# Performance work log

Measured on AMD Instinct MI355X. Metric: run time of the kernel, lower is better.

## Reference

```python
import jax, jax.numpy as jnp
import numpy as np

DMAX = 32
TEMPERATURE = 1.0

B, C, H, T, F = 2, 64, 64, 512, 64


def _windows(x, dmax):
    """x: (..., T, F) -> (..., T, dmax, F); w[..., t, d, :] = x_padded[..., t + d, :],
    where x is zero-padded with dmax-1 frames at the front of T (causal window
    covering frames t-dmax+1 .. t, matching torch ZeroPad2d+Unfold)."""
    Tn = x.shape[-2]
    pad = [(0, 0)] * (x.ndim - 2) + [(dmax - 1, 0), (0, 0)]
    xp = jnp.pad(x, pad)
    idx = jnp.arange(Tn)[:, None] + jnp.arange(dmax)[None, :]  # (T, dmax)
    return xp[..., idx, :]


def setup_inputs() -> dict:
    key = jax.random.key(0)
    ks = jax.random.split(key, 8)
    return {
        "x_mic": jax.random.normal(ks[0], (B, C, T, F), dtype=jnp.float32),
        "x_ref": jax.random.normal(ks[1], (B, C, T, F), dtype=jnp.float32),
        "w_mic": jax.random.normal(ks[2], (H, C), dtype=jnp.float32) * (1.0 / np.sqrt(C)),
        "b_mic": jax.random.normal(ks[3], (H,), dtype=jnp.float32) * 0.01,
        "w_ref": jax.random.normal(ks[4], (H, C), dtype=jnp.float32) * (1.0 / np.sqrt(C)),
        "b_ref": jax.random.normal(ks[5], (H,), dtype=jnp.float32) * 0.01,
        "w_conv": jax.random.normal(ks[6], (1, H, 5, 3), dtype=jnp.float32) * (1.0 / np.sqrt(H * 15)),
        "b_conv": jax.random.normal(ks[7], (1,), dtype=jnp.float32) * 0.01,
    }


def reference(x_mic, x_ref, w_mic, b_mic, w_ref, b_ref, w_conv, b_conv):
    Bn, Cn, Tn, Fn = x_ref.shape
    # 1x1 convs == channel-mixing matmuls
    Q = jnp.einsum('bctf,hc->bhtf', x_mic, w_mic) + b_mic[None, :, None, None]
    K = jnp.einsum('bctf,hc->bhtf', x_ref, w_ref) + b_ref[None, :, None, None]
    # causal sliding windows over T: (B,H,T,dmax,F)
    Kw = _windows(K, DMAX)
    # cross-correlation scores over F: (B,H,T,dmax)
    V = jnp.einsum('bhtf,bhtdf->bhtd', Q, Kw) / jnp.sqrt(jnp.asarray(Fn, jnp.float32))
    # conv over (T, dmax): pad T top by 4 (causal), dmax both sides by 1; kernel (5,3), H->1
    Vp = jnp.pad(V, ((0, 0), (0, 0), (4, 0), (1, 1)))
    Vc = jax.lax.conv_general_dilated(
        Vp, w_conv, window_strides=(1, 1), padding='VALID',
        dimension_numbers=('NCHW', 'OIHW', 'NCHW')) + b_conv[None, :, None, None]
    # delay distribution over dmax
    A = jax.nn.softmax(Vc / TEMPERATURE, axis=-1)  # (B,1,T,dmax)
    # align reference: weighted sum over the causal window
    refw = _windows(x_ref, DMAX)  # (B,C,T,dmax,F)
    aligned = jnp.einsum('btd,bctdf->bctf', A[:, 0], refw)
    return aligned
```

## Files before the change

### kernel.cpp

```cpp
#include <hip/hip_runtime.h>
#include <hip/hip_bf16.h>

#define BB 2
#define CC 64
#define HH 64
#define TT 512
#define FF 64
#define DD 32

typedef short short8 __attribute__((ext_vector_type(8)));
typedef float f32x4  __attribute__((ext_vector_type(4)));

__device__ __forceinline__ unsigned short f2bf(float x) {
    union { float f; unsigned u; } v; v.f = x;
    unsigned r = v.u + 0x7FFFu + ((v.u >> 16) & 1u);
    return (unsigned short)(r >> 16);
}

__global__ __launch_bounds__(256) void k_qk(
    const float* __restrict__ x_mic, const float* __restrict__ x_ref,
    const float* __restrict__ w_mic, const float* __restrict__ b_mic,
    const float* __restrict__ w_ref, const float* __restrict__ b_ref,
    unsigned short* __restrict__ Qb, unsigned short* __restrict__ Kb)
{
    __shared__ unsigned short Wl[64 * 72];
    __shared__ unsigned short Xt[2][64 * 72];
    __shared__ float Bs[64];

    const int tid = threadIdx.x;
    const int b   = blockIdx.x >> 8;
    const int t0  = (blockIdx.x & 255) * 2;
    const int which = blockIdx.y;

    const float* xsrc = which ? x_ref : x_mic;
    const float* wsrc = which ? w_ref : w_mic;
    const float* bsrc = which ? b_ref : b_mic;
    unsigned short* outb = which ? Kb : Qb;

    const int l  = tid & 63;
    const int w  = tid >> 6;
    const int q  = l >> 4;
    const int f4i = l & 15;

    {
        const float4* wg = reinterpret_cast<const float4*>(wsrc);
        const int h  = tid >> 2;
        #pragma unroll
        for (int p = 0; p < 4; ++p) {
            const int c0 = (tid & 3) * 4 + p * 16;
            float4 wv = wg[h * 16 + (c0 >> 2)];
            unsigned w0 = (unsigned)f2bf(wv.x) | ((unsigned)f2bf(wv.y) << 16);
            unsigned w1 = (unsigned)f2bf(wv.z) | ((unsigned)f2bf(wv.w) << 16);
            uint2* dst = reinterpret_cast<uint2*>(&Wl[h * 72 + c0]);
            *dst = make_uint2(w0, w1);
        }
    }
    if (tid < 64) Bs[tid] = bsrc[tid];

    {
        const float4* xg = reinterpret_cast<const float4*>(
            xsrc + (size_t)b * CC * TT * FF);
        #pragma unroll
        for (int t = 0; t < 2; ++t) {
            #pragma unroll
            for (int p = 0; p < 4; ++p) {
                const int cbase = p * 16 + 4 * w;
                const int c     = cbase + q;
                float4 xv = xg[((size_t)c * TT + (t0 + t)) * 16 + f4i];
                float v0 = xv.x, v1 = xv.y, v2 = xv.z, v3 = xv.w;
                float s01 = __shfl_xor((q & 1) ? v0 : v1, 16);
                float s23 = __shfl_xor((q & 1) ? v2 : v3, 16);
                float w0 = (q & 1) ? s01 : v0;
                float w1 = (q & 1) ? v1  : s01;
                float w2 = (q & 1) ? s23 : v2;
                float w3 = (q & 1) ? v3  : s23;
                float r02 = __shfl_xor((q & 2) ? w0 : w2, 32);
                float r13 = __shfl_xor((q & 2) ? w1 : w3, 32);
                float u0 = (q & 2) ? r02 : w0;
                float u1 = (q & 2) ? r13 : w1;
                float u2 = (q & 2) ? w2  : r02;
                float u3 = (q & 2) ? w3  : r13;
                unsigned a0 = (unsigned)f2bf(u0) | ((unsigned)f2bf(u1) << 16);
                unsigned a1 = (unsigned)f2bf(u2) | ((unsigned)f2bf(u3) << 16);
                uint2* dst = reinterpret_cast<uint2*>(
                    &Xt[t][(4 * f4i + q) * 72 + cbase]);
                *dst = make_uint2(a0, a1);
            }
        }
    }
    __syncthreads();

    short8 a0 = *reinterpret_cast<const short8*>(&Wl[(16 * w + f4i) * 72 + q * 8]);
    short8 a1 = *reinterpret_cast<const short8*>(&Wl[(16 * w + f4i) * 72 + (4 + q) * 8]);

    #pragma unroll
    for (int t = 0; t < 2; ++t) {
        f32x4 acc[4];
        #pragma unroll
        for (int n = 0; n < 4; ++n) acc[n] = (f32x4){0.f, 0.f, 0.f, 0.f};

        #pragma unroll
        for (int n = 0; n < 4; ++n) {
            short8 b0 = *reinterpret_cast<const short8*>(
                &Xt[t][(16 * n + f4i) * 72 + q * 8]);
            short8 b1 = *reinterpret_cast<const short8*>(
                &Xt[t][(16 * n + f4i) * 72 + (4 + q) * 8]);
            acc[n] = __builtin_amdgcn_mfma_f32_16x16x32_bf16(a0, b0, acc[n], 0, 0, 0);
            acc[n] = __builtin_amdgcn_mfma_f32_16x16x32_bf16(a1, b1, acc[n], 0, 0, 0);
        }
        #pragma unroll
        for (int n = 0; n < 4; ++n) {
            #pragma unroll
            for (int r = 0; r < 4; ++r) {
                const int h = 16 * w + 4 * q + r;
                const int f = 16 * n + f4i;
                float val = acc[n][r] + Bs[h];
                outb[((size_t)(b * HH + h) * TT + (t0 + t)) * FF + f] = f2bf(val);
            }
        }
    }
}

__global__ __launch_bounds__(256) void k_scores(
    const unsigned short* __restrict__ Qb, const unsigned short* __restrict__ Kb,
    float* __restrict__ V)
{
    __shared__ unsigned short Ql[64 * 72];
    __shared__ unsigned short Kl[96 * 72];

    const int tid = threadIdx.x;
    const int t0  = blockIdx.x * 64;
    const int h   = blockIdx.y, b = blockIdx.z;

    const size_t base = ((size_t)(b * HH + h) * TT) * FF;

    #pragma unroll
    for (int it = 0; it < 5; ++it) {
        int idx = it * 256 + tid;
        if (idx < 512) {
            int r = idx >> 3, g = idx & 7;
            uint4 v = *reinterpret_cast<const uint4*>(Qb + base + (size_t)(t0 + r) * FF + g * 8);
            *reinterpret_cast<uint4*>(&Ql[r * 72 + g * 8]) = v;
        } else {
            int idx2 = idx - 512;
            int r = idx2 >> 3, g = idx2 & 7;
            int j = t0 - 31 + r;
            uint4 v = make_uint4(0u, 0u, 0u, 0u);
            if (j >= 0 && j < TT)
                v = *reinterpret_cast<const uint4*>(Kb + base + (size_t)j * FF + g * 8);
            *reinterpret_cast<uint4*>(&Kl[r * 72 + g * 8]) = v;
        }
    }
    __syncthreads();

    const int l = tid & 63;
    const int w = tid >> 6;
    const int q = l >> 4;
    const int nl = l & 15;

    short8 a0 = *reinterpret_cast<const short8*>(&Ql[(16 * w + nl) * 72 + q * 8]);
    short8 a1 = *reinterpret_cast<const short8*>(&Ql[(16 * w + nl) * 72 + (4 + q) * 8]);

    f32x4 acc[3];
    #pragma unroll
    for (int n = 0; n < 3; ++n) acc[n] = (f32x4){0.f, 0.f, 0.f, 0.f};

    #pragma unroll
    for (int n = 0; n < 3; ++n) {
        short8 b0 = *reinterpret_cast<const short8*>(
            &Kl[(16 * w + 16 * n + nl) * 72 + q * 8]);
        short8 b1 = *reinterpret_cast<const short8*>(
            &Kl[(16 * w + 16 * n + nl) * 72 + (4 + q) * 8]);
        acc[n] = __builtin_amdgcn_mfma_f32_16x16x32_bf16(a0, b0, acc[n], 0, 0, 0);
        acc[n] = __builtin_amdgcn_mfma_f32_16x16x32_bf16(a1, b1, acc[n], 0, 0, 0);
    }

    #pragma unroll
    for (int n = 0; n < 3; ++n) {
        #pragma unroll
        for (int r = 0; r < 4; ++r) {
            const int tloc = 16 * w + 4 * q + r;
            const int d = 16 * n + nl - 4 * q - r;
            if (d >= 0 && d < DD) {
                const int t = t0 + tloc;
                V[((size_t)(b * TT + t) * HH + h) * DD + d] = acc[n][r] * 0.125f;
            }
        }
    }
}

__global__ __launch_bounds__(256) void k_conv_softmax(
    const float* __restrict__ V, const float* __restrict__ wconv,
    const float* __restrict__ bconv, float* __restrict__ A)
{
    __shared__ float Vs[4 + 5 * 2048 + 4];
    __shared__ float wcs[960];
    __shared__ float parts[8 * 32];

    const int tid = threadIdx.x;
    const int t = blockIdx.x, b = blockIdx.y;

    #pragma unroll
    for (int idx = tid; idx < 960; idx += 256) wcs[idx] = wconv[idx];

    const float4* vg = reinterpret_cast<const float4*>(V);
    float4* vs4 = reinterpret_cast<float4*>(Vs);
    #pragma unroll
    for (int idx = tid; idx < 5 * 512; idx += 256) {
        int i = idx >> 9, f4i = idx & 511;
        int tt = t - 4 + i;
        float4 v = make_float4(0.f, 0.f, 0.f, 0.f);
        if (tt >= 0) v = vg[((size_t)(b * TT) + tt) * 512 + f4i];
        vs4[1 + idx] = v;
    }
    __syncthreads();

    const int d  = tid & 31;
    const int hg = tid >> 5;
    float s = 0.f;
    #pragma unroll
    for (int i = 0; i < 5; ++i) {
        #pragma unroll
        for (int hh = 0; hh < 8; ++hh) {
            int h = hg * 8 + hh;
            int base = 4 + i * 2048 + h * 32 + d;
            float vm = Vs[base - 1];  vm = (d > 0)  ? vm : 0.f;
            float v0 = Vs[base];
            float vp = Vs[base + 1];  vp = (d < 31) ? vp : 0.f;
            const float* wr = &wcs[h * 15 + i * 3];
            s += vm * wr[0] + v0 * wr[1] + vp * wr[2];
        }
    }
    parts[hg * 32 + d] = s;
    __syncthreads();

    if (tid < 32) {
        float vc = bconv[0];
        #pragma unroll
        for (int g = 0; g < 8; ++g) vc += parts[g * 32 + tid];
        float m = vc;
        #pragma unroll
        for (int off = 16; off >= 1; off >>= 1) m = fmaxf(m, __shfl_xor(m, off));
        float e = __expf(vc - m);
        float ssum = e;
        #pragma unroll
        for (int off = 16; off >= 1; off >>= 1) ssum += __shfl_xor(ssum, off);
        A[((size_t)(b * TT) + t) * DD + tid] = e / ssum;
    }
}

__global__ __launch_bounds__(256) void k_align(
    const float* __restrict__ x_ref, const float* __restrict__ A, float* __restrict__ out)
{
    __shared__ float Xs[63 * 68];
    __shared__ float As[32 * 33];

    const int tid = threadIdx.x;
    const int t0  = blockIdx.x * 32;
    const int c   = blockIdx.y, b = blockIdx.z;

    const float4* xg = reinterpret_cast<const float4*>(
        x_ref + ((size_t)(b * CC + c) * TT) * FF);
    float4* xs4 = reinterpret_cast<float4*>(Xs);
    #pragma unroll
    for (int idx = tid; idx < 63 * 16; idx += 256) {
        int r = idx >> 4, f4 = idx & 15;
        int tt = t0 - 31 + r;
        float4 v = make_float4(0.f, 0.f, 0.f, 0.f);
        if (tt >= 0) v = xg[tt * 16 + f4];
        xs4[r * 17 + f4] = v;
    }
    #pragma unroll
    for (int idx = tid; idx < 32 * 32; idx += 256) {
        int i = idx >> 5, d = idx & 31;
        As[i * 33 + d] = A[((size_t)(b * TT) + t0 + i) * DD + d];
    }
    __syncthreads();

    const int f4 = tid & 15;
    const int i0 = tid >> 4;
    float4* out4 = reinterpret_cast<float4*>(out);

    #pragma unroll
    for (int pass = 0; pass < 2; ++pass) {
        const int i = i0 + pass * 16;
        float ax = 0.f, ay = 0.f, az = 0.f, aw = 0.f;
        #pragma unroll 8
        for (int d = 0; d < 32; ++d) {
            float a = As[i * 33 + d];
            float4 x = xs4[(i + d) * 17 + f4];
            ax += a * x.x; ay += a * x.y; az += a * x.z; aw += a * x.w;
        }
        out4[((size_t)(b * CC + c) * TT + t0 + i) * 16 + f4] =
            make_float4(ax, ay, az, aw);
    }
}

extern "C" void kernel_launch(void* const* d_in, const int* in_sizes, int n_in,
                              void* d_out, int out_size, void* d_ws, size_t ws_size,
                              hipStream_t stream)
{
    const float* x_mic  = (const float*)d_in[0];
    const float* x_ref  = (const float*)d_in[1];
    const float* w_mic  = (const float*)d_in[2];
    const float* b_mic  = (const float*)d_in[3];
    const float* w_ref  = (const float*)d_in[4];
    const float* b_ref  = (const float*)d_in[5];
    const float* w_conv = (const float*)d_in[6];
    const float* b_conv = (const float*)d_in[7];
    float* out = (float*)d_out;

    unsigned short* Qb = (unsigned short*)d_ws;
    unsigned short* Kb = Qb + 4194304;
    float* V = (float*)(Kb + 4194304);
    float* A = V + 2097152;

    k_qk<<<dim3(BB * (TT / 2), 2), 256, 0, stream>>>(
        x_mic, x_ref, w_mic, b_mic, w_ref, b_ref, Qb, Kb);
    k_scores<<<dim3(TT / 64, HH, BB), 256, 0, stream>>>(Qb, Kb, V);
    k_conv_softmax<<<dim3(TT, BB), 256, 0, stream>>>(V, w_conv, b_conv, A);
    k_align<<<dim3(TT / 32, CC, BB), 256, 0, stream>>>(x_ref, A, out);
}
```

Baseline: 131.8 us.

## Rework QK store layout, batch conv-softmax over timesteps, register-block align kernel

The QK projection now swaps the MFMA operands so each lane holds four consecutive features of one head, which allows packed 8-byte bf16 stores in place of scattered 2-byte stores. Conv+softmax processes four timesteps per block with a padded shared layout, float4 reads, shuffle-based neighbour access and a wave-level reduction, so each block reuses the 8 loaded V rows and drops the second barrier. The align kernel moves to 64-timestep tiles and builds a banded weight matrix in shared memory, so each thread computes a 4x4 register block and the x_ref window reads are amortised. These changes add shared memory use and extra setup for the banded weights, which may lower occupancy.

```diff
diff --git a/kernel.cpp b/kernel.cpp
--- a/kernel.cpp
+++ b/kernel.cpp
@@ -40,7 +40,7 @@
     const int l  = tid & 63;
     const int w  = tid >> 6;
     const int q  = l >> 4;
-    const int f4i = l & 15;
+    const int nl = l & 15;
 
     {
         const float4* wg = reinterpret_cast<const float4*>(wsrc);
@@ -66,7 +66,7 @@
             for (int p = 0; p < 4; ++p) {
                 const int cbase = p * 16 + 4 * w;
                 const int c     = cbase + q;
-                float4 xv = xg[((size_t)c * TT + (t0 + t)) * 16 + f4i];
+                float4 xv = xg[((size_t)c * TT + (t0 + t)) * 16 + nl];
                 float v0 = xv.x, v1 = xv.y, v2 = xv.z, v3 = xv.w;
                 float s01 = __shfl_xor((q & 1) ? v0 : v1, 16);
                 float s23 = __shfl_xor((q & 1) ? v2 : v3, 16);
@@ -83,40 +83,34 @@
                 unsigned a0 = (unsigned)f2bf(u0) | ((unsigned)f2bf(u1) << 16);
                 unsigned a1 = (unsigned)f2bf(u2) | ((unsigned)f2bf(u3) << 16);
                 uint2* dst = reinterpret_cast<uint2*>(
-                    &Xt[t][(4 * f4i + q) * 72 + cbase]);
+                    &Xt[t][(4 * nl + q) * 72 + cbase]);
                 *dst = make_uint2(a0, a1);
             }
         }
     }
     __syncthreads();
 
-    short8 a0 = *reinterpret_cast<const short8*>(&Wl[(16 * w + f4i) * 72 + q * 8]);
-    short8 a1 = *reinterpret_cast<const short8*>(&Wl[(16 * w + f4i) * 72 + (4 + q) * 8]);
+    short8 b0 = *reinterpret_cast<const short8*>(&Wl[(16 * w + nl) * 72 + q * 8]);
+    short8 b1 = *reinterpret_cast<const short8*>(&Wl[(16 * w + nl) * 72 + (4 + q) * 8]);
+    const int h = 16 * w + nl;
+    const float bv = Bs[h];
 
     #pragma unroll
     for (int t = 0; t < 2; ++t) {
-        f32x4 acc[4];
-        #pragma unroll
-        for (int n = 0; n < 4; ++n) acc[n] = (f32x4){0.f, 0.f, 0.f, 0.f};
-
-        #pragma unroll
-        for (int n = 0; n < 4; ++n) {
-            short8 b0 = *reinterpret_cast<const short8*>(
-                &Xt[t][(16 * n + f4i) * 72 + q * 8]);
-            short8 b1 = *reinterpret_cast<const short8*>(
-                &Xt[t][(16 * n + f4i) * 72 + (4 + q) * 8]);
-            acc[n] = __builtin_amdgcn_mfma_f32_16x16x32_bf16(a0, b0, acc[n], 0, 0, 0);
-            acc[n] = __builtin_amdgcn_mfma_f32_16x16x32_bf16(a1, b1, acc[n], 0, 0, 0);
-        }
-        #pragma unroll
-        for (int n = 0; n < 4; ++n) {
-            #pragma unroll
-            for (int r = 0; r < 4; ++r) {
-                const int h = 16 * w + 4 * q + r;
-                const int f = 16 * n + f4i;
-                float val = acc[n][r] + Bs[h];
-                outb[((size_t)(b * HH + h) * TT + (t0 + t)) * FF + f] = f2bf(val);
-            }
+        #pragma unroll
+        for (int mt = 0; mt < 4; ++mt) {
+            f32x4 acc = (f32x4){0.f, 0.f, 0.f, 0.f};
+            short8 a0 = *reinterpret_cast<const short8*>(
+                &Xt[t][(16 * mt + nl) * 72 + q * 8]);
+            short8 a1 = *reinterpret_cast<const short8*>(
+                &Xt[t][(16 * mt + nl) * 72 + (4 + q) * 8]);
+            acc = __builtin_amdgcn_mfma_f32_16x16x32_bf16(a0, b0, acc, 0, 0, 0);
+            acc = __builtin_amdgcn_mfma_f32_16x16x32_bf16(a1, b1, acc, 0, 0, 0);
+            unsigned lo = (unsigned)f2bf(acc[0] + bv) | ((unsigned)f2bf(acc[1] + bv) << 16);
+            unsigned hi = (unsigned)f2bf(acc[2] + bv) | ((unsigned)f2bf(acc[3] + bv) << 16);
+            uint2* dst = reinterpret_cast<uint2*>(
+                &outb[((size_t)(b * HH + h) * TT + (t0 + t)) * FF + 16 * mt + 4 * q]);
+            *dst = make_uint2(lo, hi);
         }
     }
 }
@@ -193,107 +187,153 @@
     const float* __restrict__ V, const float* __restrict__ wconv,
     const float* __restrict__ bconv, float* __restrict__ A)
 {
-    __shared__ float Vs[4 + 5 * 2048 + 4];
+    __shared__ float Vs[8 * 2304];
     __shared__ float wcs[960];
-    __shared__ float parts[8 * 32];
 
     const int tid = threadIdx.x;
-    const int t = blockIdx.x, b = blockIdx.y;
+    const int t0 = blockIdx.x * 4, b = blockIdx.y;
 
     #pragma unroll
     for (int idx = tid; idx < 960; idx += 256) wcs[idx] = wconv[idx];
 
     const float4* vg = reinterpret_cast<const float4*>(V);
-    float4* vs4 = reinterpret_cast<float4*>(Vs);
-    #pragma unroll
-    for (int idx = tid; idx < 5 * 512; idx += 256) {
-        int i = idx >> 9, f4i = idx & 511;
-        int tt = t - 4 + i;
+    #pragma unroll
+    for (int it = 0; it < 16; ++it) {
+        int idx = it * 256 + tid;
+        int r = idx >> 9, g = idx & 511;
+        int h = g >> 3, d4 = g & 7;
+        int tt = t0 - 4 + r;
         float4 v = make_float4(0.f, 0.f, 0.f, 0.f);
-        if (tt >= 0) v = vg[((size_t)(b * TT) + tt) * 512 + f4i];
-        vs4[1 + idx] = v;
-    }
-    __syncthreads();
-
-    const int d  = tid & 31;
-    const int hg = tid >> 5;
-    float s = 0.f;
+        if (tt >= 0) v = vg[((size_t)(b * TT) + tt) * 512 + g];
+        *reinterpret_cast<float4*>(&Vs[r * 2304 + h * 36 + d4 * 4]) = v;
+    }
+    __syncthreads();
+
+    const int dq = tid & 7;
+    const int hg = (tid >> 3) & 7;
+    const int tt = tid >> 6;
+
+    float px = 0.f, py = 0.f, pz = 0.f, pw = 0.f;
     #pragma unroll
     for (int i = 0; i < 5; ++i) {
+        const int r = tt + i;
         #pragma unroll
         for (int hh = 0; hh < 8; ++hh) {
-            int h = hg * 8 + hh;
-            int base = 4 + i * 2048 + h * 32 + d;
-            float vm = Vs[base - 1];  vm = (d > 0)  ? vm : 0.f;
-            float v0 = Vs[base];
-            float vp = Vs[base + 1];  vp = (d < 31) ? vp : 0.f;
-            const float* wr = &wcs[h * 15 + i * 3];
-            s += vm * wr[0] + v0 * wr[1] + vp * wr[2];
-        }
-    }
-    parts[hg * 32 + d] = s;
-    __syncthreads();
-
-    if (tid < 32) {
-        float vc = bconv[0];
-        #pragma unroll
-        for (int g = 0; g < 8; ++g) vc += parts[g * 32 + tid];
-        float m = vc;
-        #pragma unroll
-        for (int off = 16; off >= 1; off >>= 1) m = fmaxf(m, __shfl_xor(m, off));
-        float e = __expf(vc - m);
-        float ssum = e;
-        #pragma unroll
-        for (int off = 16; off >= 1; off >>= 1) ssum += __shfl_xor(ssum, off);
-        A[((size_t)(b * TT) + t) * DD + tid] = e / ssum;
+            const int h = hg + 8 * hh;
+            float4 cur = *reinterpret_cast<const float4*>(
+                &Vs[r * 2304 + h * 36 + dq * 4]);
+            float pv = __shfl_up(cur.w, 1);
+            float nx = __shfl_down(cur.x, 1);
+            if (dq == 0) pv = 0.f;
+            if (dq == 7) nx = 0.f;
+            const float w0 = wcs[h * 15 + i * 3 + 0];
+            const float w1 = wcs[h * 15 + i * 3 + 1];
+            const float w2 = wcs[h * 15 + i * 3 + 2];
+            px += w0 * pv    + w1 * cur.x + w2 * cur.y;
+            py += w0 * cur.x + w1 * cur.y + w2 * cur.z;
+            pz += w0 * cur.y + w1 * cur.z + w2 * cur.w;
+            pw += w0 * cur.z + w1 * cur.w + w2 * nx;
+        }
+    }
+    #pragma unroll
+    for (int off = 8; off <= 32; off <<= 1) {
+        px += __shfl_xor(px, off);
+        py += __shfl_xor(py, off);
+        pz += __shfl_xor(pz, off);
+        pw += __shfl_xor(pw, off);
+    }
+    const float bc = bconv[0];
+    px += bc; py += bc; pz += bc; pw += bc;
+    float m = fmaxf(fmaxf(px, py), fmaxf(pz, pw));
+    #pragma unroll
+    for (int off = 1; off <= 4; off <<= 1) m = fmaxf(m, __shfl_xor(m, off));
+    float ex = __expf(px - m), ey = __expf(py - m);
+    float ez = __expf(pz - m), ew = __expf(pw - m);
+    float s = ex + ey + ez + ew;
+    #pragma unroll
+    for (int off = 1; off <= 4; off <<= 1) s += __shfl_xor(s, off);
+    const float inv = 1.f / s;
+    if (hg == 0) {
+        const int t = t0 + tt;
+        float4 av = make_float4(ex * inv, ey * inv, ez * inv, ew * inv);
+        *reinterpret_cast<float4*>(&A[((size_t)(b * TT) + t) * DD + 4 * dq]) = av;
     }
 }
 
 __global__ __launch_bounds__(256) void k_align(
     const float* __restrict__ x_ref, const float* __restrict__ A, float* __restrict__ out)
 {
-    __shared__ float Xs[63 * 68];
-    __shared__ float As[32 * 33];
+    __shared__ float Xs[95 * 68];
+    __shared__ float As[64 * 36];
+    __shared__ float Ap[16 * 37 * 4];
 
     const int tid = threadIdx.x;
-    const int t0  = blockIdx.x * 32;
+    const int t0  = blockIdx.x * 64;
     const int c   = blockIdx.y, b = blockIdx.z;
 
     const float4* xg = reinterpret_cast<const float4*>(
         x_ref + ((size_t)(b * CC + c) * TT) * FF);
     float4* xs4 = reinterpret_cast<float4*>(Xs);
     #pragma unroll
-    for (int idx = tid; idx < 63 * 16; idx += 256) {
-        int r = idx >> 4, f4 = idx & 15;
-        int tt = t0 - 31 + r;
-        float4 v = make_float4(0.f, 0.f, 0.f, 0.f);
-        if (tt >= 0) v = xg[tt * 16 + f4];
-        xs4[r * 17 + f4] = v;
-    }
-    #pragma unroll
-    for (int idx = tid; idx < 32 * 32; idx += 256) {
-        int i = idx >> 5, d = idx & 31;
-        As[i * 33 + d] = A[((size_t)(b * TT) + t0 + i) * DD + d];
+    for (int it = 0; it < 6; ++it) {
+        int idx = it * 256 + tid;
+        if (idx < 95 * 16) {
+            int r = idx >> 4, f4 = idx & 15;
+            int tt = t0 - 31 + r;
+            float4 v = make_float4(0.f, 0.f, 0.f, 0.f);
+            if (tt >= 0) v = xg[tt * 16 + f4];
+            xs4[r * 17 + f4] = v;
+        }
+    }
+    #pragma unroll
+    for (int it = 0; it < 2; ++it) {
+        int idx = it * 256 + tid;
+        int i = idx >> 3, d4 = idx & 7;
+        *reinterpret_cast<float4*>(&As[i * 36 + 4 * d4]) =
+            *reinterpret_cast<const float4*>(&A[((size_t)(b * TT) + t0 + i) * DD + 4 * d4]);
+    }
+    __syncthreads();
+    #pragma unroll
+    for (int it = 0; it < 3; ++it) {
+        int idx = it * 256 + tid;
+        if (idx < 16 * 37) {
+            int bi = idx / 37, rr = idx - bi * 37;
+            float wv[4];
+            #pragma unroll
+            for (int r = 0; r < 4; ++r) {
+                int d = rr - r;
+                wv[r] = (d >= 0 && d < 32) ? As[(4 * bi + r) * 36 + d] : 0.f;
+            }
+            float4* dst = reinterpret_cast<float4*>(&Ap[(bi * 37 + rr) * 4]);
+            *dst = make_float4(wv[0], wv[1], wv[2], wv[3]);
+        }
     }
     __syncthreads();
 
     const int f4 = tid & 15;
-    const int i0 = tid >> 4;
-    float4* out4 = reinterpret_cast<float4*>(out);
-
-    #pragma unroll
-    for (int pass = 0; pass < 2; ++pass) {
-        const int i = i0 + pass * 16;
-        float ax = 0.f, ay = 0.f, az = 0.f, aw = 0.f;
-        #pragma unroll 8
-        for (int d = 0; d < 32; ++d) {
-            float a = As[i * 33 + d];
-            float4 x = xs4[(i + d) * 17 + f4];
-            ax += a * x.x; ay += a * x.y; az += a * x.z; aw += a * x.w;
-        }
-        out4[((size_t)(b * CC + c) * TT + t0 + i) * 16 + f4] =
-            make_float4(ax, ay, az, aw);
-    }
+    const int bi = tid >> 4;
+
+    float4 acc0 = make_float4(0.f, 0.f, 0.f, 0.f);
+    float4 acc1 = make_float4(0.f, 0.f, 0.f, 0.f);
+    float4 acc2 = make_float4(0.f, 0.f, 0.f, 0.f);
+    float4 acc3 = make_float4(0.f, 0.f, 0.f, 0.f);
+
+    #pragma unroll 7
+    for (int rr = 0; rr < 35; ++rr) {
+        float4 W4 = *reinterpret_cast<const float4*>(&Ap[(bi * 37 + rr) * 4]);
+        float4 X4 = xs4[(4 * bi + rr) * 17 + f4];
+        acc0.x += W4.x * X4.x; acc0.y += W4.x * X4.y; acc0.z += W4.x * X4.z; acc0.w += W4.x * X4.w;
+        acc1.x += W4.y * X4.x; acc1.y += W4.y * X4.y; acc1.z += W4.y * X4.z; acc1.w += W4.y * X4.w;
+        acc2.x += W4.z * X4.x; acc2.y += W4.z * X4.y; acc2.z += W4.z * X4.z; acc2.w += W4.z * X4.w;
+        acc3.x += W4.w * X4.x; acc3.y += W4.w * X4.y; acc3.z += W4.w * X4.z; acc3.w += W4.w * X4.w;
+    }
+
+    float4* o4 = reinterpret_cast<float4*>(out);
+    const size_t obase = ((size_t)(b * CC + c) * TT + t0 + 4 * bi) * 16 + f4;
+    o4[obase +  0] = acc0;
+    o4[obase + 16] = acc1;
+    o4[obase + 32] = acc2;
+    o4[obase + 48] = acc3;
 }
 
 extern "C" void kernel_launch(void* const* d_in, const int* in_sizes, int n_in,
@@ -318,6 +358,6 @@
     k_qk<<<dim3(BB * (TT / 2), 2), 256, 0, stream>>>(
         x_mic, x_ref, w_mic, b_mic, w_ref, b_ref, Qb, Kb);
     k_scores<<<dim3(TT / 64, HH, BB), 256, 0, stream>>>(Qb, Kb, V);
-    k_conv_softmax<<<dim3(TT, BB), 256, 0, stream>>>(V, w_conv, b_conv, A);
-    k_align<<<dim3(TT / 32, CC, BB), 256, 0, stream>>>(x_ref, A, out);
-}
+    k_conv_softmax<<<dim3(TT / 4, BB), 256, 0, stream>>>(V, w_conv, b_conv, A);
+    k_align<<<dim3(TT / 64, CC, BB), 256, 0, stream>>>(x_ref, A, out);
+}
```

New measurement: 125.7 us (median of 2 runs). 1.05x faster.
